# Optimization experiments

Measured on AMD Instinct MI355X. Metric: run time of the kernel, lower is better.

Reference implementation:

```python
import jax, jax.numpy as jnp
import numpy as np
from jax import lax

B, T, D, H, L, W = 256, 1024, 32, 64, 32, 64
DT0 = 0.4  # fixed dt0 in _sample


def _u(key, shape, fan_in):
    lim = 1.0 / np.sqrt(fan_in)
    return jax.random.uniform(key, shape, dtype=jnp.float32, minval=-lim, maxval=lim)


def setup_inputs() -> dict:
    key = jax.random.key(0)
    ks = jax.random.split(key, 32)
    inp = {}
    inp['ts'] = jnp.sort(jax.random.uniform(ks[0], (B, T), dtype=jnp.float32) * 10.0, axis=1)
    inp['ys'] = jax.random.normal(ks[1], (B, T, D), dtype=jnp.float32)
    inp['eps'] = jax.random.normal(ks[2], (B, L), dtype=jnp.float32)
    inp['scale'] = jnp.ones(())
    # Func MLP: H -> W -> W -> H, softplus hidden acts, tanh final
    inp['fw0'] = _u(ks[3], (W, H), H); inp['fb0'] = _u(ks[4], (W,), H)
    inp['fw1'] = _u(ks[5], (W, W), W); inp['fb1'] = _u(ks[6], (W,), W)
    inp['fw2'] = _u(ks[7], (H, W), W); inp['fb2'] = _u(ks[8], (H,), W)
    # GRUCell: input D+1 (time concat), hidden H (equinox layout)
    inp['gru_wi'] = _u(ks[9], (3 * H, D + 1), D + 1)
    inp['gru_wh'] = _u(ks[10], (3 * H, H), H)
    inp['gru_b'] = _u(ks[11], (3 * H,), H)
    inp['gru_bn'] = _u(ks[12], (H,), H)
    inp['hl_w'] = _u(ks[13], (2 * L, H), H); inp['hl_b'] = _u(ks[14], (2 * L,), H)
    # latent_to_hidden MLP: L -> W -> W -> H, relu hidden (equinox default), identity final
    inp['lh_w0'] = _u(ks[15], (W, L), L); inp['lh_b0'] = _u(ks[16], (W,), L)
    inp['lh_w1'] = _u(ks[17], (W, W), W); inp['lh_b1'] = _u(ks[18], (W,), W)
    inp['lh_w2'] = _u(ks[19], (H, W), W); inp['lh_b2'] = _u(ks[20], (H,), W)
    inp['hd_w'] = _u(ks[21], (D, H), H); inp['hd_b'] = _u(ks[22], (D,), H)
    return inp


def _forward(ts, ys, eps, scale, fw0, fb0, fw1, fb1, fw2, fb2,
             gru_wi, gru_wh, gru_b, gru_bn, hl_w, hl_b,
             lh_w0, lh_b0, lh_w1, lh_b1, lh_w2, lh_b2, hd_w, hd_b):
    Bv, Tlen = ts.shape
    Hv = gru_wh.shape[1]
    Lv = hl_w.shape[0] // 2

    # ---- encoder: GRU over reversed (t, y) sequence ----
    data = jnp.concatenate([ts[..., None], ys], axis=-1)    # [B,T,D+1]
    data_rev = jnp.swapaxes(data[:, ::-1, :], 0, 1)          # [T,B,D+1]

    def gru_step(h, x):
        ig = x @ gru_wi.T + gru_b                            # [B,3H]
        hg = h @ gru_wh.T                                    # [B,3H]
        ir, iz, inn = jnp.split(ig, 3, axis=-1)
        hr, hz, hn = jnp.split(hg, 3, axis=-1)
        r = jax.nn.sigmoid(ir + hr)
        z = jax.nn.sigmoid(iz + hz)
        n = jnp.tanh(inn + r * (hn + gru_bn))
        return n + z * (h - n), None

    hidden, _ = lax.scan(gru_step, jnp.zeros((Bv, Hv), data.dtype), data_rev)

    context = hidden @ hl_w.T + hl_b                         # [B,2L]
    mean, logstd = context[:, :Lv], context[:, Lv:]
    std = jnp.exp(logstd)
    latent = mean + eps * std                                # reparameterized sample

    # ---- latent -> initial hidden state (relu MLP) ----
    h0 = jax.nn.relu(latent @ lh_w0.T + lh_b0)
    h0 = jax.nn.relu(h0 @ lh_w1.T + lh_b1)
    y0 = h0 @ lh_w2.T + lh_b2                                # [B,H]

    def func(y):  # Func: scale * mlp(y); softplus hidden, tanh final
        a = jax.nn.softplus(y @ fw0.T + fb0)
        a = jax.nn.softplus(a @ fw1.T + fb1)
        return scale * jnp.tanh(a @ fw2.T + fb2)

    # ---- Euler integrator over T steps (vector field is time-independent) ----
    def euler_step(carry, _):
        t0, y = carry
        y1 = y + DT0 * func(y)
        return (t0 + DT0, y1), y1

    (_, _), ys_h = lax.scan(euler_step, (ts[:, 0], y0), None, length=Tlen)  # [T,B,H]
    pred_ys = jnp.swapaxes(ys_h @ hd_w.T + hd_b, 0, 1)       # [B,T,D]

    # ---- ELBO-style loss, per sample ----
    recon = 0.5 * jnp.sum((ys - pred_ys) ** 2, axis=(1, 2))
    kl = 0.5 * jnp.sum(mean ** 2 + std ** 2 - 2.0 * jnp.log(std) - 1.0, axis=1)
    return recon + kl                                         # [B]


def reference(ts, ys, eps, scale, fw0, fb0, fw1, fb1, fw2, fb2,
              gru_wi, gru_wh, gru_b, gru_bn, hl_w, hl_b,
              lh_w0, lh_b0, lh_w1, lh_b1, lh_w2, lh_b2, hd_w, hd_b):
    return _forward(ts, ys, eps, scale, fw0, fb0, fw1, fb1, fw2, fb2,
                    gru_wi, gru_wh, gru_b, gru_bn, hl_w, hl_b,
                    lh_w0, lh_b0, lh_w1, lh_b1, lh_w2, lh_b2, hd_w, hd_b)
```

## Files before the change

kernel.cpp:

```cpp
#include <hip/hip_runtime.h>
#include <math.h>

#define NB 256
#define NT 1024
#define ND 32
#define NH 64
#define NL 32
#define DT0 0.4f
#define XB 36

__device__ __forceinline__ float dot4(float4 a, float4 b) {
    return a.x * b.x + a.y * b.y + a.z * b.z + a.w * b.w;
}
__device__ __forceinline__ float fsigm(float x) {
    return __fdividef(1.0f, 1.0f + __expf(-x));
}
__device__ __forceinline__ float ftanh(float x) {
    float cx = fminf(fmaxf(x, -15.0f), 15.0f);
    float e2 = __expf(2.0f * cx);
    return __fdividef(e2 - 1.0f, e2 + 1.0f);
}
__device__ __forceinline__ float fsoftplus(float x) {
    return fmaxf(x, 0.0f) + __logf(1.0f + __expf(-fabsf(x)));
}

template <int CTRL>
__device__ __forceinline__ float dpp_add(float x) {
    int t = __builtin_amdgcn_update_dpp(0, __float_as_int(x), CTRL, 0xF, 0xF, true);
    return x + __int_as_float(t);
}
__device__ __forceinline__ float quad_reduce(float x) {
    x = dpp_add<0xB1>(x);
    x = dpp_add<0x4E>(x);
    return x;
}

extern "C" __global__ void __launch_bounds__(256, 1)
latentode_fused(const float* __restrict__ ts,
                const float* __restrict__ ys,
                const float* __restrict__ eps,
                const float* __restrict__ scale_p,
                const float* __restrict__ fw0, const float* __restrict__ fb0,
                const float* __restrict__ fw1, const float* __restrict__ fb1,
                const float* __restrict__ fw2, const float* __restrict__ fb2,
                const float* __restrict__ gwi, const float* __restrict__ gwh,
                const float* __restrict__ gb,  const float* __restrict__ gbn,
                const float* __restrict__ hlw, const float* __restrict__ hlb,
                const float* __restrict__ lw0, const float* __restrict__ lb0,
                const float* __restrict__ lw1, const float* __restrict__ lb1,
                const float* __restrict__ lw2, const float* __restrict__ lb2,
                const float* __restrict__ hdw, const float* __restrict__ hdb,
                float* __restrict__ out)
{
    const int b   = blockIdx.x;
    const int tid = threadIdx.x;
    const int w   = tid >> 6;
    const int ln  = tid & 63;

    __shared__ __align__(16) float xb[NT * XB];
    __shared__ __align__(16) float hbuf[2][64];
    __shared__ __align__(16) float a0b[64];
    __shared__ __align__(16) float a1b[64];
    __shared__ __align__(16) float tmpb[64];
    __shared__ __align__(16) float ybuf[64];
    __shared__ __align__(16) float latb[32];
    __shared__ float redr[32];

    for (int i = tid; i < NT * 8; i += 256) {
        const int row = i >> 3, q = i & 7;
        *(float4*)&xb[row * XB + q * 4] =
            *(const float4*)(ys + (size_t)(b * NT + row) * ND + q * 4);
    }
    for (int i = tid; i < NT; i += 256) xb[i * XB + 32] = ts[b * NT + i];

    const int u = (w << 4) + (ln >> 2);
    const int p = ln & 3;
    const float4* whr = (const float4*)(gwh + (u)       * 64 + p * 16);
    const float4* whz = (const float4*)(gwh + (64 + u)  * 64 + p * 16);
    const float4* whn = (const float4*)(gwh + (128 + u) * 64 + p * 16);
    const float4 WR0=whr[0], WR1=whr[1], WR2=whr[2], WR3=whr[3];
    const float4 WZ0=whz[0], WZ1=whz[1], WZ2=whz[2], WZ3=whz[3];
    const float4 WN0=whn[0], WN1=whn[1], WN2=whn[2], WN3=whn[3];
    const float* gr = gwi + u * 33;
    const float* gz = gwi + (64 + u) * 33;
    const float* gn = gwi + (128 + u) * 33;
    const int o = 8 * p;
    const float4 RIA = make_float4(gr[1+o], gr[2+o], gr[3+o], gr[4+o]);
    const float4 RIB = make_float4(gr[5+o], gr[6+o], gr[7+o], gr[8+o]);
    const float4 ZIA = make_float4(gz[1+o], gz[2+o], gz[3+o], gz[4+o]);
    const float4 ZIB = make_float4(gz[5+o], gz[6+o], gz[7+o], gz[8+o]);
    const float4 NIA = make_float4(gn[1+o], gn[2+o], gn[3+o], gn[4+o]);
    const float4 NIB = make_float4(gn[5+o], gn[6+o], gn[7+o], gn[8+o]);
    const float RT  = (p == 0) ? gr[0] : 0.0f;
    const float ZT  = (p == 0) ? gz[0] : 0.0f;
    const float NTW = (p == 0) ? gn[0] : 0.0f;
    const float gbr_ = gb[u], gbz_ = gb[64 + u], gbn_ = gb[128 + u];
    const float bnv  = gbn[u];

    if (tid < 64) hbuf[0][tid] = 0.0f;
    __syncthreads();

    float hreg = 0.0f;
    float4 xA = *(const float4*)(&xb[0] + o);
    float4 xB = *(const float4*)(&xb[0] + o + 4);
    float tsv = xb[32];
    for (int s = 0; s < NT; ++s) {
        const int sn = (s + 1 < NT) ? (s + 1) : s;
        const float* xrown = &xb[sn * XB];
        const float4 nxA = *(const float4*)(xrown + o);
        const float4 nxB = *(const float4*)(xrown + o + 4);
        const float ntsv = xrown[32];

        const float4* hv = (const float4*)&hbuf[s & 1][p * 16];
        const float4 h0 = hv[0], h1 = hv[1], h2 = hv[2], h3 = hv[3];

        float ar = dot4(WR0,h0) + dot4(WR1,h1) + dot4(WR2,h2) + dot4(WR3,h3)
                 + dot4(RIA,xA) + dot4(RIB,xB) + RT * tsv;
        float az = dot4(WZ0,h0) + dot4(WZ1,h1) + dot4(WZ2,h2) + dot4(WZ3,h3)
                 + dot4(ZIA,xA) + dot4(ZIB,xB) + ZT * tsv;
        float ahn = dot4(WN0,h0) + dot4(WN1,h1) + dot4(WN2,h2) + dot4(WN3,h3);
        float ain = dot4(NIA,xA) + dot4(NIB,xB) + NTW * tsv;

        ar  = quad_reduce(ar);
        az  = quad_reduce(az);
        ahn = quad_reduce(ahn);
        ain = quad_reduce(ain);

        const float rg = fsigm(ar + gbr_);
        const float zg = fsigm(az + gbz_);
        const float ng = ftanh(ain + gbn_ + rg * (ahn + bnv));
        hreg = ng + zg * (hreg - ng);
        if (p == 0) hbuf[(s + 1) & 1][u] = hreg;
        xA = nxA; xB = nxB; tsv = ntsv;
        __syncthreads();
    }

    if (tid < 64) {
        const float4* wp = (const float4*)(hlw + tid * 64);
        const float4* hv = (const float4*)&hbuf[0][0];
        float a0 = hlb[tid], a1 = 0.0f;
#pragma unroll
        for (int q = 0; q < 16; q += 2) { a0 += dot4(wp[q], hv[q]); a1 += dot4(wp[q+1], hv[q+1]); }
        tmpb[tid] = a0 + a1;
    }
    __syncthreads();
    float klpart = 0.0f;
    if (tid < 32) {
        const float mean   = tmpb[tid];
        const float logstd = tmpb[32 + tid];
        const float stdv   = __expf(logstd);
        latb[tid] = mean + eps[b * NL + tid] * stdv;
        klpart = 0.5f * (mean * mean + stdv * stdv - 2.0f * logstd - 1.0f);
    }
    __syncthreads();
    if (tid < 64) {
        const float4* wp = (const float4*)(lw0 + tid * 32);
        const float4* lv = (const float4*)latb;
        float a0 = lb0[tid], a1 = 0.0f;
#pragma unroll
        for (int q = 0; q < 8; q += 2) { a0 += dot4(wp[q], lv[q]); a1 += dot4(wp[q+1], lv[q+1]); }
        a0b[tid] = fmaxf(a0 + a1, 0.0f);
    }
    __syncthreads();
    if (tid < 64) {
        const float4* wp = (const float4*)(lw1 + tid * 64);
        const float4* av = (const float4*)a0b;
        float a0 = lb1[tid], a1 = 0.0f;
#pragma unroll
        for (int q = 0; q < 16; q += 2) { a0 += dot4(wp[q], av[q]); a1 += dot4(wp[q+1], av[q+1]); }
        a1b[tid] = fmaxf(a0 + a1, 0.0f);
    }
    __syncthreads();
    if (tid < 64) {
        const float4* wp = (const float4*)(lw2 + tid * 64);
        const float4* tv = (const float4*)a1b;
        float a0 = lb2[tid], a1 = 0.0f;
#pragma unroll
        for (int q = 0; q < 16; q += 2) { a0 += dot4(wp[q], tv[q]); a1 += dot4(wp[q+1], tv[q+1]); }
        ybuf[tid] = a0 + a1;
    }
    __syncthreads();

    const int er = tid >> 2, ep = tid & 3;
    const float4* q0 = (const float4*)(fw0 + er * 64 + ep * 16);
    const float4 E00=q0[0], E01=q0[1], E02=q0[2], E03=q0[3];
    const float4* q1 = (const float4*)(fw1 + er * 64 + ep * 16);
    const float4 E10=q1[0], E11=q1[1], E12=q1[2], E13=q1[3];
    const float4* q2 = (const float4*)(fw2 + er * 64 + ep * 16);
    const float4 E20=q2[0], E21=q2[1], E22=q2[2], E23=q2[3];
    const float b0 = fb0[er], b1 = fb1[er], b2 = fb2[er];
    const int hr2 = tid >> 3, hp = tid & 7;
    const float4* qh = (const float4*)(hdw + hr2 * 64 + hp * 8);
    const float4 HD0 = qh[0], HD1 = qh[1];
    const float hdbias = hdb[hr2];
    const float dts = DT0 * scale_p[0];
    float ylocal = (ep == 0) ? ybuf[er] : 0.0f;
    float rec = 0.0f;

    for (int s = 0; s < NT; ++s) {
        {
            const float4* yv = (const float4*)ybuf;
            float l0 = dot4(E00, yv[ep*4+0]) + dot4(E01, yv[ep*4+1])
                     + dot4(E02, yv[ep*4+2]) + dot4(E03, yv[ep*4+3]);
            l0 = quad_reduce(l0);
            if (ep == 0) a0b[er] = fsoftplus(l0 + b0);
        }
        __syncthreads();
        {
            const float4* av = (const float4*)a0b;
            float l1 = dot4(E10, av[ep*4+0]) + dot4(E11, av[ep*4+1])
                     + dot4(E12, av[ep*4+2]) + dot4(E13, av[ep*4+3]);
            l1 = quad_reduce(l1);

            const float4* yv = (const float4*)ybuf;
            float ph = dot4(HD0, yv[hp*2+0]) + dot4(HD1, yv[hp*2+1]);
            ph = quad_reduce(ph);
            ph = dpp_add<0x104>(ph);
            if (ep == 0) a1b[er] = fsoftplus(l1 + b1);
            if (hp == 0 && s > 0) {
                const float d = xb[(s - 1) * XB + hr2] - (ph + hdbias);
                rec += d * d;
            }
        }
        __syncthreads();
        {
            const float4* bv = (const float4*)a1b;
            float l2 = dot4(E20, bv[ep*4+0]) + dot4(E21, bv[ep*4+1])
                     + dot4(E22, bv[ep*4+2]) + dot4(E23, bv[ep*4+3]);
            l2 = quad_reduce(l2);
            if (ep == 0) {
                ylocal += dts * ftanh(l2 + b2);
                ybuf[er] = ylocal;
            }
        }
        __syncthreads();
    }

    {
        const float4* yv = (const float4*)ybuf;
        float ph = dot4(HD0, yv[hp*2+0]) + dot4(HD1, yv[hp*2+1]);
        ph = quad_reduce(ph);
        ph = dpp_add<0x104>(ph);
        if (hp == 0) {
            const float d = xb[(NT - 1) * XB + hr2] - (ph + hdbias);
            rec += d * d;
            redr[hr2] = rec;
        }
    }
    float klv = klpart;
    klv += __shfl_xor(klv, 1);
    klv += __shfl_xor(klv, 2);
    klv += __shfl_xor(klv, 4);
    klv += __shfl_xor(klv, 8);
    klv += __shfl_xor(klv, 16);
    __syncthreads();
    if (tid == 0) {
        float rs = 0.0f;
#pragma unroll
        for (int k2 = 0; k2 < 32; ++k2) rs += redr[k2];
        out[b] = 0.5f * rs + klv;
    }
}

extern "C" void kernel_launch(void* const* d_in, const int* in_sizes, int n_in,
                              void* d_out, int out_size, void* d_ws, size_t ws_size,
                              hipStream_t stream) {
    (void)in_sizes; (void)n_in; (void)out_size; (void)d_ws; (void)ws_size;
    const float* ts      = (const float*)d_in[0];
    const float* ys      = (const float*)d_in[1];
    const float* eps     = (const float*)d_in[2];
    const float* scale_p = (const float*)d_in[3];
    const float* fw0     = (const float*)d_in[4];
    const float* fb0     = (const float*)d_in[5];
    const float* fw1     = (const float*)d_in[6];
    const float* fb1     = (const float*)d_in[7];
    const float* fw2     = (const float*)d_in[8];
    const float* fb2     = (const float*)d_in[9];
    const float* gwi     = (const float*)d_in[10];
    const float* gwh     = (const float*)d_in[11];
    const float* gbv     = (const float*)d_in[12];
    const float* gbn     = (const float*)d_in[13];
    const float* hlw     = (const float*)d_in[14];
    const float* hlb     = (const float*)d_in[15];
    const float* lw0     = (const float*)d_in[16];
    const float* lb0     = (const float*)d_in[17];
    const float* lw1     = (const float*)d_in[18];
    const float* lb1     = (const float*)d_in[19];
    const float* lw2     = (const float*)d_in[20];
    const float* lb2     = (const float*)d_in[21];
    const float* hdw     = (const float*)d_in[22];
    const float* hdb     = (const float*)d_in[23];
    float* out = (float*)d_out;

    hipLaunchKernelGGL(latentode_fused, dim3(NB), dim3(256), 0, stream,
                       ts, ys, eps, scale_p, fw0, fb0, fw1, fb1, fw2, fb2,
                       gwi, gwh, gbv, gbn, hlw, hlb, lw0, lb0, lw1, lb1,
                       lw2, lb2, hdw, hdb, out);
}
```

Measured before the change: 1.165 ms.

## Double block size: split GRU dots across 8 lanes, move head projection to extra waves

The block grows from 256 to 512 threads. In the GRU encoder each hidden unit is now computed by 8 lanes instead of 4, so each lane has shorter dot-product chains plus one extra DPP reduction step, and only one lane per unit evaluates the gates. In the Euler decoder the output-head projection and reconstruction error move to the four new waves, so they run beside the MLP waves instead of being serialized into stage two. The cost is more waves taking part in every per-step __syncthreads barrier, and a changed final reduction of the reconstruction sum.

```diff
diff --git a/kernel.cpp b/kernel.cpp
--- a/kernel.cpp
+++ b/kernel.cpp
@@ -8,6 +8,7 @@
 #define NL 32
 #define DT0 0.4f
 #define XB 36
+#define BT 512
 
 __device__ __forceinline__ float dot4(float4 a, float4 b) {
     return a.x * b.x + a.y * b.y + a.z * b.z + a.w * b.w;
@@ -34,8 +35,14 @@
     x = dpp_add<0x4E>(x);
     return x;
 }
-
-extern "C" __global__ void __launch_bounds__(256, 1)
+__device__ __forceinline__ float red8(float x) {
+    x = dpp_add<0xB1>(x);
+    x = dpp_add<0x4E>(x);
+    x = dpp_add<0x104>(x);
+    return x;
+}
+
+extern "C" __global__ void __launch_bounds__(BT, 1)
 latentode_fused(const float* __restrict__ ts,
                 const float* __restrict__ ys,
                 const float* __restrict__ eps,
@@ -64,33 +71,30 @@
     __shared__ __align__(16) float tmpb[64];
     __shared__ __align__(16) float ybuf[64];
     __shared__ __align__(16) float latb[32];
-    __shared__ float redr[32];
-
-    for (int i = tid; i < NT * 8; i += 256) {
+    __shared__ float redr[8];
+
+    for (int i = tid; i < NT * 8; i += BT) {
         const int row = i >> 3, q = i & 7;
         *(float4*)&xb[row * XB + q * 4] =
             *(const float4*)(ys + (size_t)(b * NT + row) * ND + q * 4);
     }
-    for (int i = tid; i < NT; i += 256) xb[i * XB + 32] = ts[b * NT + i];
-
-    const int u = (w << 4) + (ln >> 2);
-    const int p = ln & 3;
-    const float4* whr = (const float4*)(gwh + (u)       * 64 + p * 16);
-    const float4* whz = (const float4*)(gwh + (64 + u)  * 64 + p * 16);
-    const float4* whn = (const float4*)(gwh + (128 + u) * 64 + p * 16);
-    const float4 WR0=whr[0], WR1=whr[1], WR2=whr[2], WR3=whr[3];
-    const float4 WZ0=whz[0], WZ1=whz[1], WZ2=whz[2], WZ3=whz[3];
-    const float4 WN0=whn[0], WN1=whn[1], WN2=whn[2], WN3=whn[3];
+    for (int i = tid; i < NT; i += BT) xb[i * XB + 32] = ts[b * NT + i];
+
+    const int u = tid >> 3;
+    const int p = tid & 7;
+    const float4* whr = (const float4*)(gwh + (u)       * 64 + p * 8);
+    const float4* whz = (const float4*)(gwh + (64 + u)  * 64 + p * 8);
+    const float4* whn = (const float4*)(gwh + (128 + u) * 64 + p * 8);
+    const float4 WR0=whr[0], WR1=whr[1];
+    const float4 WZ0=whz[0], WZ1=whz[1];
+    const float4 WN0=whn[0], WN1=whn[1];
     const float* gr = gwi + u * 33;
     const float* gz = gwi + (64 + u) * 33;
     const float* gn = gwi + (128 + u) * 33;
-    const int o = 8 * p;
+    const int o = 4 * p;
     const float4 RIA = make_float4(gr[1+o], gr[2+o], gr[3+o], gr[4+o]);
-    const float4 RIB = make_float4(gr[5+o], gr[6+o], gr[7+o], gr[8+o]);
     const float4 ZIA = make_float4(gz[1+o], gz[2+o], gz[3+o], gz[4+o]);
-    const float4 ZIB = make_float4(gz[5+o], gz[6+o], gz[7+o], gz[8+o]);
     const float4 NIA = make_float4(gn[1+o], gn[2+o], gn[3+o], gn[4+o]);
-    const float4 NIB = make_float4(gn[5+o], gn[6+o], gn[7+o], gn[8+o]);
     const float RT  = (p == 0) ? gr[0] : 0.0f;
     const float ZT  = (p == 0) ? gz[0] : 0.0f;
     const float NTW = (p == 0) ? gn[0] : 0.0f;
@@ -102,36 +106,33 @@
 
     float hreg = 0.0f;
     float4 xA = *(const float4*)(&xb[0] + o);
-    float4 xB = *(const float4*)(&xb[0] + o + 4);
     float tsv = xb[32];
     for (int s = 0; s < NT; ++s) {
         const int sn = (s + 1 < NT) ? (s + 1) : s;
-        const float* xrown = &xb[sn * XB];
-        const float4 nxA = *(const float4*)(xrown + o);
-        const float4 nxB = *(const float4*)(xrown + o + 4);
-        const float ntsv = xrown[32];
-
-        const float4* hv = (const float4*)&hbuf[s & 1][p * 16];
-        const float4 h0 = hv[0], h1 = hv[1], h2 = hv[2], h3 = hv[3];
-
-        float ar = dot4(WR0,h0) + dot4(WR1,h1) + dot4(WR2,h2) + dot4(WR3,h3)
-                 + dot4(RIA,xA) + dot4(RIB,xB) + RT * tsv;
-        float az = dot4(WZ0,h0) + dot4(WZ1,h1) + dot4(WZ2,h2) + dot4(WZ3,h3)
-                 + dot4(ZIA,xA) + dot4(ZIB,xB) + ZT * tsv;
-        float ahn = dot4(WN0,h0) + dot4(WN1,h1) + dot4(WN2,h2) + dot4(WN3,h3);
-        float ain = dot4(NIA,xA) + dot4(NIB,xB) + NTW * tsv;
-
-        ar  = quad_reduce(ar);
-        az  = quad_reduce(az);
-        ahn = quad_reduce(ahn);
-        ain = quad_reduce(ain);
-
-        const float rg = fsigm(ar + gbr_);
-        const float zg = fsigm(az + gbz_);
-        const float ng = ftanh(ain + gbn_ + rg * (ahn + bnv));
-        hreg = ng + zg * (hreg - ng);
-        if (p == 0) hbuf[(s + 1) & 1][u] = hreg;
-        xA = nxA; xB = nxB; tsv = ntsv;
+        const float4 nxA = *(const float4*)(&xb[sn * XB] + o);
+        const float ntsv = xb[sn * XB + 32];
+
+        const float4* hv = (const float4*)&hbuf[s & 1][p * 8];
+        const float4 h0 = hv[0], h1 = hv[1];
+
+        float ar  = dot4(WR0,h0) + dot4(WR1,h1) + dot4(RIA,xA) + RT * tsv;
+        float az  = dot4(WZ0,h0) + dot4(WZ1,h1) + dot4(ZIA,xA) + ZT * tsv;
+        float ahn = dot4(WN0,h0) + dot4(WN1,h1);
+        float ain = dot4(NIA,xA) + NTW * tsv;
+
+        ar  = red8(ar);
+        az  = red8(az);
+        ahn = red8(ahn);
+        ain = red8(ain);
+
+        if (p == 0) {
+            const float rg = fsigm(ar + gbr_);
+            const float zg = fsigm(az + gbz_);
+            const float ng = ftanh(ain + gbn_ + rg * (ahn + bnv));
+            hreg = ng + zg * (hreg - ng);
+            hbuf[(s + 1) & 1][u] = hreg;
+        }
+        xA = nxA; tsv = ntsv;
         __syncthreads();
     }
 
@@ -181,7 +182,8 @@
     }
     __syncthreads();
 
-    const int er = tid >> 2, ep = tid & 3;
+    const int er = (tid < 256) ? (tid >> 2) : 0;
+    const int ep = tid & 3;
     const float4* q0 = (const float4*)(fw0 + er * 64 + ep * 16);
     const float4 E00=q0[0], E01=q0[1], E02=q0[2], E03=q0[3];
     const float4* q1 = (const float4*)(fw1 + er * 64 + ep * 16);
@@ -189,41 +191,41 @@
     const float4* q2 = (const float4*)(fw2 + er * 64 + ep * 16);
     const float4 E20=q2[0], E21=q2[1], E22=q2[2], E23=q2[3];
     const float b0 = fb0[er], b1 = fb1[er], b2 = fb2[er];
-    const int hr2 = tid >> 3, hp = tid & 7;
-    const float4* qh = (const float4*)(hdw + hr2 * 64 + hp * 8);
+    const int hu = (tid >= 256) ? ((tid - 256) >> 3) : 0;
+    const int hp = tid & 7;
+    const float4* qh = (const float4*)(hdw + hu * 64 + hp * 8);
     const float4 HD0 = qh[0], HD1 = qh[1];
-    const float hdbias = hdb[hr2];
+    const float hdbias = hdb[hu];
     const float dts = DT0 * scale_p[0];
-    float ylocal = (ep == 0) ? ybuf[er] : 0.0f;
+    float ylocal = (tid < 256 && ep == 0) ? ybuf[er] : 0.0f;
     float rec = 0.0f;
 
     for (int s = 0; s < NT; ++s) {
-        {
+        if (tid < 256) {
             const float4* yv = (const float4*)ybuf;
             float l0 = dot4(E00, yv[ep*4+0]) + dot4(E01, yv[ep*4+1])
                      + dot4(E02, yv[ep*4+2]) + dot4(E03, yv[ep*4+3]);
             l0 = quad_reduce(l0);
             if (ep == 0) a0b[er] = fsoftplus(l0 + b0);
+        } else {
+            const float4* yv = (const float4*)ybuf;
+            float ph = dot4(HD0, yv[hp*2+0]) + dot4(HD1, yv[hp*2+1]);
+            ph = red8(ph);
+            if (hp == 0 && s > 0) {
+                const float d = xb[(s - 1) * XB + hu] - (ph + hdbias);
+                rec += d * d;
+            }
         }
         __syncthreads();
-        {
+        if (tid < 256) {
             const float4* av = (const float4*)a0b;
             float l1 = dot4(E10, av[ep*4+0]) + dot4(E11, av[ep*4+1])
                      + dot4(E12, av[ep*4+2]) + dot4(E13, av[ep*4+3]);
             l1 = quad_reduce(l1);
-
-            const float4* yv = (const float4*)ybuf;
-            float ph = dot4(HD0, yv[hp*2+0]) + dot4(HD1, yv[hp*2+1]);
-            ph = quad_reduce(ph);
-            ph = dpp_add<0x104>(ph);
             if (ep == 0) a1b[er] = fsoftplus(l1 + b1);
-            if (hp == 0 && s > 0) {
-                const float d = xb[(s - 1) * XB + hr2] - (ph + hdbias);
-                rec += d * d;
-            }
         }
         __syncthreads();
-        {
+        if (tid < 256) {
             const float4* bv = (const float4*)a1b;
             float l2 = dot4(E20, bv[ep*4+0]) + dot4(E21, bv[ep*4+1])
                      + dot4(E22, bv[ep*4+2]) + dot4(E23, bv[ep*4+3]);
@@ -236,16 +238,21 @@
         __syncthreads();
     }
 
-    {
+    if (tid >= 256) {
         const float4* yv = (const float4*)ybuf;
         float ph = dot4(HD0, yv[hp*2+0]) + dot4(HD1, yv[hp*2+1]);
-        ph = quad_reduce(ph);
-        ph = dpp_add<0x104>(ph);
+        ph = red8(ph);
         if (hp == 0) {
-            const float d = xb[(NT - 1) * XB + hr2] - (ph + hdbias);
+            const float d = xb[(NT - 1) * XB + hu] - (ph + hdbias);
             rec += d * d;
-            redr[hr2] = rec;
-        }
+        }
+    }
+    {
+        float rv = rec;
+        rv += __shfl_xor(rv, 8);
+        rv += __shfl_xor(rv, 16);
+        rv += __shfl_xor(rv, 32);
+        if (tid >= 256 && ln == 0) redr[w - 4] = rv;
     }
     float klv = klpart;
     klv += __shfl_xor(klv, 1);
@@ -255,9 +262,7 @@
     klv += __shfl_xor(klv, 16);
     __syncthreads();
     if (tid == 0) {
-        float rs = 0.0f;
-#pragma unroll
-        for (int k2 = 0; k2 < 32; ++k2) rs += redr[k2];
+        const float rs = redr[0] + redr[1] + redr[2] + redr[3];
         out[b] = 0.5f * rs + klv;
     }
 }
@@ -292,7 +297,7 @@
     const float* hdb     = (const float*)d_in[23];
     float* out = (float*)d_out;
 
-    hipLaunchKernelGGL(latentode_fused, dim3(NB), dim3(256), 0, stream,
+    hipLaunchKernelGGL(latentode_fused, dim3(NB), dim3(BT), 0, stream,
                        ts, ys, eps, scale_p, fw0, fb0, fw1, fb1, fw2, fb2,
                        gwi, gwh, gbv, gbn, hlw, hlb, lw0, lb0, lw1, lb1,
                        lw2, lb2, hdw, hdb, out);
```

Measured after the change: 1.197 ms. 2.7% more time.
